# Kernel tuning notes

Hardware: AMD Instinct MI355X
Metric: run time of the kernel (lower is better)

Reference implementation:

```python
import jax, jax.numpy as jnp
import numpy as np

D = 1024
H = 16
HD = D // H
S = 2048
B = 2
INNER = 4 * D
EPS = 1e-5


def _layernorm(x, w, b):
    mu = jnp.mean(x, axis=-1, keepdims=True)
    var = jnp.mean(jnp.square(x - mu), axis=-1, keepdims=True)
    return (x - mu) * jax.lax.rsqrt(var + EPS) * w + b


def _rope(x, cos, sin):
    # x: [B, S, H, HD]; cos/sin: [S, HD//2]
    xe, xo = x[..., 0::2], x[..., 1::2]
    c = cos[None, :, None, :]
    s = sin[None, :, None, :]
    oe = xe * c - xo * s
    oo = xe * s + xo * c
    return jnp.stack([oe, oo], axis=-1).reshape(x.shape)


def setup_inputs() -> dict:
    key = jax.random.key(0)
    ks = jax.random.split(key, 12)
    hidden_states = jax.random.normal(ks[0], (B, S, D), dtype=jnp.float32)
    time_step_emb = jax.random.normal(ks[1], (B, 6 * D), dtype=jnp.float32)
    # causal additive mask [1,1,S,S]
    causal = jnp.tril(jnp.ones((S, S), dtype=bool))
    attention_mask = jnp.where(causal, 0.0, -1e9).astype(jnp.float32)[None, None]
    # proper RoPE tables
    inv_freq = 1.0 / (10000.0 ** (np.arange(0, HD, 2, dtype=np.float32) / HD))
    t = np.arange(S, dtype=np.float32)
    freqs = np.outer(t, inv_freq)  # [S, HD//2]
    rope_cos = jnp.asarray(np.cos(freqs))
    rope_sin = jnp.asarray(np.sin(freqs))
    p = 0.02
    params = dict(
        ln1_w=jnp.ones((D,), jnp.float32), ln1_b=jnp.zeros((D,), jnp.float32),
        ln2_w=jnp.ones((D,), jnp.float32), ln2_b=jnp.zeros((D,), jnp.float32),
        c_attn_w=jax.random.normal(ks[2], (D, 3 * D), jnp.float32) * p,
        c_attn_b=jnp.zeros((3 * D,), jnp.float32),
        c_proj_w=jax.random.normal(ks[3], (D, D), jnp.float32) * p,
        c_proj_b=jnp.zeros((D,), jnp.float32),
        fc_w=jax.random.normal(ks[4], (D, INNER), jnp.float32) * p,
        fc_b=jnp.zeros((INNER,), jnp.float32),
        proj_w=jax.random.normal(ks[5], (INNER, D), jnp.float32) * p,
        proj_b=jnp.zeros((D,), jnp.float32),
        scale_shift_table=jax.random.normal(ks[6], (6, D), jnp.float32) / np.sqrt(D),
    )
    return dict(hidden_states=hidden_states, attention_mask=attention_mask,
                time_step_emb=time_step_emb, rope_cos=rope_cos, rope_sin=rope_sin,
                **params)


def reference(hidden_states, attention_mask, time_step_emb, rope_cos, rope_sin,
              ln1_w, ln1_b, ln2_w, ln2_b, c_attn_w, c_attn_b, c_proj_w, c_proj_b,
              fc_w, fc_b, proj_w, proj_b, scale_shift_table):
    b = hidden_states.shape[0]
    mods = scale_shift_table[None] + time_step_emb.reshape(b, 6, D)  # [B,6,D]
    sh_msa, sc_msa, g_msa, sh_mlp, sc_mlp, g_mlp = [mods[:, i:i + 1] for i in range(6)]

    residual = hidden_states
    h = _layernorm(hidden_states, ln1_w, ln1_b) * (1.0 + sc_msa) + sh_msa

    qkv = h @ c_attn_w + c_attn_b  # [B,S,3D]
    q, k, v = jnp.split(qkv, 3, axis=-1)
    q = _rope(q.reshape(b, S, H, HD), rope_cos, rope_sin)
    k = _rope(k.reshape(b, S, H, HD), rope_cos, rope_sin)
    v = v.reshape(b, S, H, HD)
    scores = jnp.einsum('bqhd,bkhd->bhqk', q, k) / np.sqrt(float(HD))
    scores = scores + attention_mask
    attn = jax.nn.softmax(scores, axis=-1)
    out = jnp.einsum('bhqk,bkhd->bqhd', attn, v).reshape(b, S, D)
    attn_out = out @ c_proj_w + c_proj_b

    hidden = attn_out * g_msa + residual
    residual = hidden
    h = _layernorm(hidden, ln2_w, ln2_b) * (1.0 + sc_mlp) + sh_mlp
    h = jax.nn.gelu(h @ fc_w + fc_b, approximate=True)  # gelu_new (tanh approx)
    h = h @ proj_w + proj_b
    return h * g_mlp + residual
```

## Files before the change

kernel.cpp:

```cpp
#include <hip/hip_runtime.h>
#include <hip/hip_bf16.h>

#define D_MODEL 1024
#define N_HEADS 16
#define HEAD_DIM 64
#define SEQ 2048
#define BATCH 2
#define INNER_DIM 4096
#define ROWS (BATCH*SEQ)

using f32x4  = __attribute__((ext_vector_type(4))) float;
using bf16x8 = __attribute__((ext_vector_type(8))) short;

__device__ __forceinline__ void gl_lds16(const void* g, void* l) {
  __builtin_amdgcn_global_load_lds(
      (const __attribute__((address_space(1))) void*)g,
      (__attribute__((address_space(3))) void*)l, 16, 0, 0);
}

__device__ __forceinline__ float bf2f(unsigned short u) {
  union { unsigned int i; float f; } v; v.i = ((unsigned int)u) << 16; return v.f;
}
__device__ __forceinline__ unsigned short f2bf(float f) {
  union { float f; unsigned int i; } v; v.f = f;
  unsigned int x = v.i;
  return (unsigned short)((x + 0x7fffu + ((x >> 16) & 1u)) >> 16);
}

__device__ __forceinline__ float exp2fast(float x) {
  return __builtin_amdgcn_exp2f(x);
}

__device__ __forceinline__ float gelu_tanh(float x) {
  float x3 = x * x * x;
  float z = 0.7978845608028654f * (x + 0.044715f * x3);
  z = fminf(z, 15.0f);
  float e = __expf(2.0f * z);
  float th = (e - 1.0f) / (e + 1.0f);
  return 0.5f * x * (1.0f + th);
}

__global__ void transpose_convert(const float* __restrict__ in,
                                  unsigned short* __restrict__ out,
                                  int K, int N) {
  __shared__ float tile[32][33];
  int n0 = blockIdx.x * 32, k0 = blockIdx.y * 32;
  int tx = threadIdx.x, ty = threadIdx.y;
#pragma unroll
  for (int i = 0; i < 4; i++)
    tile[ty + i * 8][tx] = in[(size_t)(k0 + ty + i * 8) * N + n0 + tx];
  __syncthreads();
#pragma unroll
  for (int i = 0; i < 4; i++)
    out[(size_t)(n0 + ty + i * 8) * K + k0 + tx] = f2bf(tile[tx][ty + i * 8]);
}

template<int SH_IDX, int SC_IDX>
__global__ void ln_mod_kernel(const float* __restrict__ x,
                              const float* __restrict__ lw,
                              const float* __restrict__ lb,
                              const float* __restrict__ sst,
                              const float* __restrict__ temb,
                              unsigned short* __restrict__ out) {
  int row = blockIdx.x;
  int b = row >> 11;
  int t = threadIdx.x;
  const float* xr = x + (size_t)row * D_MODEL;
  float4 v = ((const float4*)xr)[t];
  float s = v.x + v.y + v.z + v.w;
  float s2 = v.x * v.x + v.y * v.y + v.z * v.z + v.w * v.w;
#pragma unroll
  for (int o = 1; o < 64; o <<= 1) { s += __shfl_xor(s, o); s2 += __shfl_xor(s2, o); }
  __shared__ float red[8];
  int wid = t >> 6, lane = t & 63;
  if (lane == 0) { red[wid] = s; red[4 + wid] = s2; }
  __syncthreads();
  s = red[0] + red[1] + red[2] + red[3];
  s2 = red[4] + red[5] + red[6] + red[7];
  float mu = s * (1.0f / D_MODEL);
  float var = s2 * (1.0f / D_MODEL) - mu * mu;
  float rs = rsqrtf(var + 1e-5f);
  int d0 = t * 4;
  float xv[4] = { v.x, v.y, v.z, v.w };
  ushort4 ov;
  unsigned short* po = (unsigned short*)&ov;
#pragma unroll
  for (int j = 0; j < 4; j++) {
    int d = d0 + j;
    float ln = (xv[j] - mu) * rs * lw[d] + lb[d];
    float sc = sst[SC_IDX * D_MODEL + d] + temb[b * 6 * D_MODEL + SC_IDX * D_MODEL + d];
    float sh = sst[SH_IDX * D_MODEL + d] + temb[b * 6 * D_MODEL + SH_IDX * D_MODEL + d];
    po[j] = f2bf(ln * (1.0f + sc) + sh);
  }
  *((ushort4*)(out + (size_t)row * D_MODEL + d0)) = ov;
}

__global__ void rope_kernel(unsigned short* __restrict__ qkv,
                            const float* __restrict__ cosb,
                            const float* __restrict__ sinb) {
  int t = blockIdx.x * blockDim.x + threadIdx.x;
  int row = t >> 10;
  int rem = t & 1023;
  int qk = rem >> 9;
  int rem2 = rem & 511;
  int hh = rem2 >> 5;
  int i = rem2 & 31;
  int s = row & (SEQ - 1);
  unsigned int* p = (unsigned int*)(qkv + (size_t)row * 3072 + qk * 1024 + hh * 64 + 2 * i);
  unsigned int pv = *p;
  float xe = bf2f((unsigned short)(pv & 0xffff));
  float xo = bf2f((unsigned short)(pv >> 16));
  float c = cosb[s * 32 + i], sn = sinb[s * 32 + i];
  float sc = (qk == 0) ? 0.18033688011112042f : 1.0f;
  float oe = (xe * c - xo * sn) * sc;
  float oo = (xe * sn + xo * c) * sc;
  *p = (((unsigned int)f2bf(oo)) << 16) | (unsigned int)f2bf(oe);
}

enum { EPI_BF16 = 0, EPI_RES = 1, EPI_GELU = 2, EPI_FINAL = 3 };

template<int EPI, int BMF>
__global__ __launch_bounds__(256, 2)
void gemm_kernel(const unsigned short* __restrict__ A,
                 const unsigned short* __restrict__ Bt,
                 const float* __restrict__ bias,
                 void* __restrict__ Cout,
                 int N, int K,
                 const float* __restrict__ sst,
                 const float* __restrict__ temb,
                 int g_idx,
                 const float* __restrict__ res) {
  __shared__ unsigned short Alds[BMF * 32 * 32];
  __shared__ unsigned short Blds[128 * 32];
  const int t = threadIdx.x;
  const int w = t >> 6, l = t & 63;
  const int lg = l >> 4, ll = l & 15;
  const int wm = w >> 1, wn = w & 1;
  const int m0 = blockIdx.y * (BMF * 32), n0 = blockIdx.x * 128;

  f32x4 acc[BMF][4] = {};

  for (int k0 = 0; k0 < K; k0 += 32) {
#pragma unroll
    for (int i = 0; i < BMF / 2; i++) {
      int c = i * 256 + t;
      int row = c >> 2, ch = c & 3;
      gl_lds16(A + (size_t)(m0 + row) * K + k0 + ch * 8, (char*)Alds + c * 16);
    }
#pragma unroll
    for (int i = 0; i < 2; i++) {
      int c = i * 256 + t;
      int row = c >> 2, ch = c & 3;
      gl_lds16(Bt + (size_t)(n0 + row) * K + k0 + ch * 8, (char*)Blds + c * 16);
    }
    __syncthreads();
    bf16x8 af[BMF], bfr[4];
#pragma unroll
    for (int mf = 0; mf < BMF; mf++)
      af[mf] = *(const bf16x8*)((const char*)Alds + (wm * (BMF * 16) + mf * 16 + ll) * 64 + lg * 16);
#pragma unroll
    for (int nf = 0; nf < 4; nf++)
      bfr[nf] = *(const bf16x8*)((const char*)Blds + (wn * 64 + nf * 16 + ll) * 64 + lg * 16);
#pragma unroll
    for (int mf = 0; mf < BMF; mf++)
#pragma unroll
      for (int nf = 0; nf < 4; nf++)
        acc[mf][nf] = __builtin_amdgcn_mfma_f32_16x16x32_bf16(af[mf], bfr[nf], acc[mf][nf], 0, 0, 0);
    __syncthreads();
  }

#pragma unroll
  for (int mf = 0; mf < BMF; mf++) {
#pragma unroll
    for (int nf = 0; nf < 4; nf++) {
      int col = n0 + wn * 64 + nf * 16 + ll;
      float bv = bias[col];
#pragma unroll
      for (int r = 0; r < 4; r++) {
        int row = m0 + wm * (BMF * 16) + mf * 16 + lg * 4 + r;
        float v = acc[mf][nf][r] + bv;
        if constexpr (EPI == EPI_BF16) {
          ((unsigned short*)Cout)[(size_t)row * N + col] = f2bf(v);
        } else if constexpr (EPI == EPI_GELU) {
          ((unsigned short*)Cout)[(size_t)row * N + col] = f2bf(gelu_tanh(v));
        } else {
          int bb = row >> 11;
          float g = sst[g_idx * D_MODEL + col] + temb[bb * 6 * D_MODEL + g_idx * D_MODEL + col];
          ((float*)Cout)[(size_t)row * N + col] = v * g + res[(size_t)row * N + col];
        }
      }
    }
  }
}

__global__ __launch_bounds__(256, 4)
void attn_kernel(const unsigned short* __restrict__ qkv,
                 unsigned short* __restrict__ attn_o) {
  __shared__ unsigned short Klds[2][64 * 64];
  __shared__ unsigned short Vt[2][64 * 64];
  __shared__ unsigned short Plds[4][16 * 64];

  const int id = blockIdx.x;
  const int bh = id & 31;
  const int b = bh >> 4, h = bh & 15;
  const int q0 = (id >> 5) * 64;
  const int t = threadIdx.x;
  const int w = t >> 6, l = t & 63;
  const int lg = l >> 4, ll = l & 15;
  const int qw0 = q0 + w * 16;
  const int q_lane = qw0 + ll;

  bf16x8 qf[2];
  {
    const unsigned short* qb = qkv + (size_t)(b * SEQ + q_lane) * 3072 + h * 64;
    qf[0] = *(const bf16x8*)(qb + lg * 8);
    qf[1] = *(const bf16x8*)(qb + 32 + lg * 8);
  }

  const int kp = t & 31, dg = t >> 5;

  f32x4 oacc[4] = {};
  float mrun = -1e30f, lrun = 0.0f;

  {
#pragma unroll
    for (int i = 0; i < 2; i++) {
      int c = i * 256 + t;
      int kr = c >> 3, cc = c & 7;
      gl_lds16(qkv + (size_t)(b * SEQ + kr) * 3072 + 1024 + h * 64 + (cc ^ (kr & 7)) * 8,
               (char*)&Klds[0][0] + c * 16);
    }
    const unsigned short* vp = qkv + (size_t)(b * SEQ + 2 * kp) * 3072 + 2048 + h * 64 + dg * 8;
    union { uint4 u; unsigned short s[8]; } a0, a1;
    a0.u = *(const uint4*)vp;
    a1.u = *(const uint4*)(vp + 3072);
    unsigned int* vt32 = (unsigned int*)&Vt[0][0];
#pragma unroll
    for (int i = 0; i < 8; i++)
      vt32[(dg * 8 + i) * 32 + (((kp >> 2) ^ i) << 2) + (kp & 3)] =
          (unsigned int)a0.s[i] | ((unsigned int)a1.s[i] << 16);
  }
  __syncthreads();

  int buf = 0;
  for (int k0 = 0; k0 <= q0; k0 += 64) {
    const bool has_next = (k0 + 64 <= q0);
    union { uint4 u; unsigned short s[8]; } n0, n1;
    if (has_next) {
#pragma unroll
      for (int i = 0; i < 2; i++) {
        int c = i * 256 + t;
        int kr = c >> 3, cc = c & 7;
        gl_lds16(qkv + (size_t)(b * SEQ + k0 + 64 + kr) * 3072 + 1024 + h * 64 + (cc ^ (kr & 7)) * 8,
                 (char*)&Klds[buf ^ 1][0] + c * 16);
      }
      const unsigned short* vp =
          qkv + (size_t)(b * SEQ + k0 + 64 + 2 * kp) * 3072 + 2048 + h * 64 + dg * 8;
      n0.u = *(const uint4*)vp;
      n1.u = *(const uint4*)(vp + 3072);
    }

    f32x4 s[4] = {};
#pragma unroll
    for (int kk = 0; kk < 2; kk++) {
#pragma unroll
      for (int nf = 0; nf < 4; nf++) {
        int key = nf * 16 + ll;
        int cc = (kk * 4 + lg) ^ (key & 7);
        bf16x8 kf = *(const bf16x8*)((const char*)&Klds[buf][0] + key * 128 + cc * 16);
        s[nf] = __builtin_amdgcn_mfma_f32_16x16x32_bf16(kf, qf[kk], s[nf], 0, 0, 0);
      }
    }
    if (k0 == q0) {
#pragma unroll
      for (int nf = 0; nf < 4; nf++) {
        int key = k0 + nf * 16 + lg * 4;
#pragma unroll
        for (int r = 0; r < 4; r++)
          if (key + r > q_lane) s[nf][r] = -1e30f;
      }
    }
    float mx = -1e30f;
#pragma unroll
    for (int nf = 0; nf < 4; nf++)
#pragma unroll
      for (int r = 0; r < 4; r++) mx = fmaxf(mx, s[nf][r]);
    mx = fmaxf(mx, __shfl_xor(mx, 16));
    mx = fmaxf(mx, __shfl_xor(mx, 32));
    float mnew = fmaxf(mrun, mx);
    float alpha = exp2fast(mrun - mnew);
    mrun = mnew;
    float ps = 0.0f;
#pragma unroll
    for (int nf = 0; nf < 4; nf++)
#pragma unroll
      for (int r = 0; r < 4; r++) {
        float p = exp2fast(s[nf][r] - mnew);
        s[nf][r] = p;
        ps += p;
      }
    ps += __shfl_xor(ps, 16);
    ps += __shfl_xor(ps, 32);
    lrun = lrun * alpha + ps;
#pragma unroll
    for (int nf = 0; nf < 4; nf++)
#pragma unroll
      for (int r = 0; r < 4; r++) oacc[nf][r] *= alpha;

#pragma unroll
    for (int nf = 0; nf < 4; nf++) {
      unsigned int lo = (unsigned int)f2bf(s[nf][0]) | ((unsigned int)f2bf(s[nf][1]) << 16);
      unsigned int hi = (unsigned int)f2bf(s[nf][2]) | ((unsigned int)f2bf(s[nf][3]) << 16);
      int chunk = (nf * 2 + (lg >> 1)) ^ (ll & 7);
      uint2 pv; pv.x = lo; pv.y = hi;
      *(uint2*)((char*)&Plds[w][0] + ll * 128 + chunk * 16 + (lg & 1) * 8) = pv;
    }
    bf16x8 pb[2];
#pragma unroll
    for (int kk = 0; kk < 2; kk++) {
      int pc = (kk * 4 + lg) ^ (ll & 7);
      pb[kk] = *(const bf16x8*)((char*)&Plds[w][0] + ll * 128 + pc * 16);
    }
#pragma unroll
    for (int nf = 0; nf < 4; nf++) {
      int d = nf * 16 + ll;
#pragma unroll
      for (int kk = 0; kk < 2; kk++) {
        int vc = (kk * 4 + lg) ^ (d & 7);
        bf16x8 vb = *(const bf16x8*)((const char*)&Vt[buf][0] + d * 128 + vc * 16);
        oacc[nf] = __builtin_amdgcn_mfma_f32_16x16x32_bf16(vb, pb[kk], oacc[nf], 0, 0, 0);
      }
    }
    if (has_next) {
      unsigned int* vt32 = (unsigned int*)&Vt[buf ^ 1][0];
#pragma unroll
      for (int i = 0; i < 8; i++)
        vt32[(dg * 8 + i) * 32 + (((kp >> 2) ^ i) << 2) + (kp & 3)] =
            (unsigned int)n0.s[i] | ((unsigned int)n1.s[i] << 16);
    }
    __syncthreads();
    buf ^= 1;
  }

  float rl = 1.0f / lrun;
#pragma unroll
  for (int nf = 0; nf < 4; nf++) {
    ushort4 ov;
    ov.x = f2bf(oacc[nf][0] * rl);
    ov.y = f2bf(oacc[nf][1] * rl);
    ov.z = f2bf(oacc[nf][2] * rl);
    ov.w = f2bf(oacc[nf][3] * rl);
    *(ushort4*)(attn_o + (size_t)(b * SEQ + q_lane) * D_MODEL + h * 64 + nf * 16 + lg * 4) = ov;
  }
}

extern "C" void kernel_launch(void* const* d_in, const int* in_sizes, int n_in,
                              void* d_out, int out_size, void* d_ws, size_t ws_size,
                              hipStream_t stream) {
  const float* hidden_states = (const float*)d_in[0];
  const float* temb     = (const float*)d_in[2];
  const float* rope_cos = (const float*)d_in[3];
  const float* rope_sin = (const float*)d_in[4];
  const float* ln1_w    = (const float*)d_in[5];
  const float* ln1_b    = (const float*)d_in[6];
  const float* ln2_w    = (const float*)d_in[7];
  const float* ln2_b    = (const float*)d_in[8];
  const float* c_attn_w = (const float*)d_in[9];
  const float* c_attn_b = (const float*)d_in[10];
  const float* c_proj_w = (const float*)d_in[11];
  const float* c_proj_b = (const float*)d_in[12];
  const float* fc_w     = (const float*)d_in[13];
  const float* fc_b     = (const float*)d_in[14];
  const float* proj_w   = (const float*)d_in[15];
  const float* proj_b   = (const float*)d_in[16];
  const float* sst      = (const float*)d_in[17];

  char* ws = (char*)d_ws;
  unsigned short* wqkv  = (unsigned short*)(ws + 0);
  unsigned short* wproj = (unsigned short*)(ws + 6291456);
  unsigned short* wfc   = (unsigned short*)(ws + 8388608);
  unsigned short* wp2   = (unsigned short*)(ws + 16777216);
  unsigned short* hln   = (unsigned short*)(ws + 25165824);
  unsigned short* qkvb  = (unsigned short*)(ws + 33554432);
  unsigned short* attno = (unsigned short*)(ws + 58720256);
  unsigned short* h3    = (unsigned short*)(ws + 33554432);
  float*          hidden = (float*)(ws + 67108864);

  dim3 tb(32, 8);
  transpose_convert<<<dim3(3072 / 32, 1024 / 32), tb, 0, stream>>>(c_attn_w, wqkv, 1024, 3072);
  transpose_convert<<<dim3(1024 / 32, 1024 / 32), tb, 0, stream>>>(c_proj_w, wproj, 1024, 1024);
  transpose_convert<<<dim3(4096 / 32, 1024 / 32), tb, 0, stream>>>(fc_w, wfc, 1024, 4096);
  transpose_convert<<<dim3(1024 / 32, 4096 / 32), tb, 0, stream>>>(proj_w, wp2, 4096, 1024);

  ln_mod_kernel<0, 1><<<ROWS, 256, 0, stream>>>(hidden_states, ln1_w, ln1_b, sst, temb, hln);

  gemm_kernel<EPI_BF16, 4><<<dim3(3072 / 128, ROWS / 128), 256, 0, stream>>>(
      hln, wqkv, c_attn_b, qkvb, 3072, 1024, nullptr, nullptr, 0, nullptr);

  rope_kernel<<<(ROWS * 1024) / 256, 256, 0, stream>>>(qkvb, rope_cos, rope_sin);

  attn_kernel<<<dim3(32 * 32), 256, 0, stream>>>(qkvb, attno);

  gemm_kernel<EPI_RES, 2><<<dim3(1024 / 128, ROWS / 64), 256, 0, stream>>>(
      attno, wproj, c_proj_b, hidden, 1024, 1024, sst, temb, 2, hidden_states);

  ln_mod_kernel<3, 4><<<ROWS, 256, 0, stream>>>(hidden, ln2_w, ln2_b, sst, temb, hln);

  gemm_kernel<EPI_GELU, 4><<<dim3(4096 / 128, ROWS / 128), 256, 0, stream>>>(
      hln, wfc, fc_b, h3, 4096, 1024, nullptr, nullptr, 0, nullptr);

  gemm_kernel<EPI_FINAL, 2><<<dim3(1024 / 128, ROWS / 64), 256, 0, stream>>>(
      h3, wp2, proj_b, d_out, 1024, 4096, sst, temb, 5, hidden);
}
```

Measured before the change: 286.6 us.

## Double-buffer GEMM LDS loads with swizzle and grouped block remap

The GEMM kernel now double-buffers its A and B LDS tiles. The next K-slice is issued via global_load_lds before the current one is computed, with manual vmcnt waits and raw barriers in place of __syncthreads. It also XOR-swizzles the 16-byte chunks within each row to reduce LDS bank conflicts on the fragment reads. Workgroup IDs are remapped so that groups of consecutive blocks share tiles for better L2 reuse. LDS usage doubles, which may reduce occupancy, and the hard-coded vmcnt counts must match the number of issued loads.

```diff
diff --git a/kernel.cpp b/kernel.cpp
--- a/kernel.cpp
+++ b/kernel.cpp
@@ -130,43 +130,74 @@
                  const float* __restrict__ temb,
                  int g_idx,
                  const float* __restrict__ res) {
-  __shared__ unsigned short Alds[BMF * 32 * 32];
-  __shared__ unsigned short Blds[128 * 32];
+  __shared__ unsigned short Alds[2][BMF * 32 * 32];
+  __shared__ unsigned short Blds[2][128 * 32];
   const int t = threadIdx.x;
   const int w = t >> 6, l = t & 63;
   const int lg = l >> 4, ll = l & 15;
   const int wm = w >> 1, wn = w & 1;
-  const int m0 = blockIdx.y * (BMF * 32), n0 = blockIdx.x * 128;
+
+  const int nx = gridDim.x;
+  const int nwg = nx * gridDim.y;
+  const int lid = blockIdx.y * nx + blockIdx.x;
+  const int nid = (lid & 7) * (nwg >> 3) + (lid >> 3);
+  const int m0 = (nid / nx) * (BMF * 32), n0 = (nid % nx) * 128;
 
   f32x4 acc[BMF][4] = {};
 
-  for (int k0 = 0; k0 < K; k0 += 32) {
+  auto stage = [&](int k0, int buf) {
 #pragma unroll
     for (int i = 0; i < BMF / 2; i++) {
       int c = i * 256 + t;
       int row = c >> 2, ch = c & 3;
-      gl_lds16(A + (size_t)(m0 + row) * K + k0 + ch * 8, (char*)Alds + c * 16);
+      int chs = ch ^ ((row >> 1) & 3);
+      gl_lds16(A + (size_t)(m0 + row) * K + k0 + chs * 8, (char*)&Alds[buf][0] + c * 16);
     }
 #pragma unroll
     for (int i = 0; i < 2; i++) {
       int c = i * 256 + t;
       int row = c >> 2, ch = c & 3;
-      gl_lds16(Bt + (size_t)(n0 + row) * K + k0 + ch * 8, (char*)Blds + c * 16);
-    }
-    __syncthreads();
+      int chs = ch ^ ((row >> 1) & 3);
+      gl_lds16(Bt + (size_t)(n0 + row) * K + k0 + chs * 8, (char*)&Blds[buf][0] + c * 16);
+    }
+  };
+
+  stage(0, 0);
+  int buf = 0;
+  for (int k0 = 0; k0 < K; k0 += 32) {
+    const bool hn = (k0 + 32 < K);
+    if (hn) {
+      stage(k0 + 32, buf ^ 1);
+      if constexpr (BMF == 4) asm volatile("s_waitcnt vmcnt(4)" ::: "memory");
+      else                    asm volatile("s_waitcnt vmcnt(3)" ::: "memory");
+    } else {
+      asm volatile("s_waitcnt vmcnt(0)" ::: "memory");
+    }
+    __builtin_amdgcn_s_barrier();
+    asm volatile("" ::: "memory");
+
     bf16x8 af[BMF], bfr[4];
 #pragma unroll
-    for (int mf = 0; mf < BMF; mf++)
-      af[mf] = *(const bf16x8*)((const char*)Alds + (wm * (BMF * 16) + mf * 16 + ll) * 64 + lg * 16);
-#pragma unroll
-    for (int nf = 0; nf < 4; nf++)
-      bfr[nf] = *(const bf16x8*)((const char*)Blds + (wn * 64 + nf * 16 + ll) * 64 + lg * 16);
+    for (int mf = 0; mf < BMF; mf++) {
+      int row = wm * (BMF * 16) + mf * 16 + ll;
+      int ch = lg ^ ((row >> 1) & 3);
+      af[mf] = *(const bf16x8*)((const char*)&Alds[buf][0] + row * 64 + ch * 16);
+    }
+#pragma unroll
+    for (int nf = 0; nf < 4; nf++) {
+      int row = wn * 64 + nf * 16 + ll;
+      int ch = lg ^ ((row >> 1) & 3);
+      bfr[nf] = *(const bf16x8*)((const char*)&Blds[buf][0] + row * 64 + ch * 16);
+    }
 #pragma unroll
     for (int mf = 0; mf < BMF; mf++)
 #pragma unroll
       for (int nf = 0; nf < 4; nf++)
         acc[mf][nf] = __builtin_amdgcn_mfma_f32_16x16x32_bf16(af[mf], bfr[nf], acc[mf][nf], 0, 0, 0);
-    __syncthreads();
+
+    asm volatile("" ::: "memory");
+    __builtin_amdgcn_s_barrier();
+    buf ^= 1;
   }
 
 #pragma unroll
```

New measurement: 283.8 us. No clear change (-1.0%).
